# Kernel optimization log

Measured on AMD Instinct MI355X. Metric: run time of the kernel, lower is better.

## Reference

```python
import jax, jax.numpy as jnp
import numpy as np

N = 100000   # nodes
E = 1600000  # edges (before self loops)
H = 4        # heads
C = 32       # per-head channels
D = H * C    # hidden_dim = 128
G = 64       # graphs in batch
L = 4        # num_layers
IN_DIM = 7
NEG_SLOPE = 0.2


def setup_inputs() -> dict:
    key = jax.random.key(0)
    ks = jax.random.split(key, 14)
    s = 0.1
    x = jax.random.normal(ks[0], (N, IN_DIM), jnp.float32)
    edge_index = jax.random.randint(ks[1], (2, E), 0, N, dtype=jnp.int32)
    batch = jnp.sort(jax.random.randint(ks[2], (N,), 0, G, dtype=jnp.int32))
    W0 = jax.random.normal(ks[3], (IN_DIM, D), jnp.float32) * s
    a_src0 = jax.random.normal(ks[4], (H, C), jnp.float32) * s
    a_dst0 = jax.random.normal(ks[5], (H, C), jnp.float32) * s
    b0 = jnp.zeros((D,), jnp.float32)
    Ws = jax.random.normal(ks[6], (L - 1, D, D), jnp.float32) * s
    a_srcs = jax.random.normal(ks[7], (L - 1, H, C), jnp.float32) * s
    a_dsts = jax.random.normal(ks[8], (L - 1, H, C), jnp.float32) * s
    bs = jnp.zeros((L - 1, D), jnp.float32)
    ln_g = jnp.ones((L, D), jnp.float32)
    ln_b = jnp.zeros((L, D), jnp.float32)
    return dict(x=x, edge_index=edge_index, batch=batch, W0=W0, a_src0=a_src0,
                a_dst0=a_dst0, b0=b0, Ws=Ws, a_srcs=a_srcs, a_dsts=a_dsts,
                bs=bs, ln_g=ln_g, ln_b=ln_b)


def _gat_layer(x, W, a_src, a_dst, b, src, dst):
    # x: [N, F_in] -> h: [N, H, C] (PyG GATConv: shared lin for src/dst)
    h = (x @ W).reshape(N, H, C)
    alpha_src = jnp.einsum('nhc,hc->nh', h, a_src)  # [N, H]
    alpha_dst = jnp.einsum('nhc,hc->nh', h, a_dst)  # [N, H]
    logits = jax.nn.leaky_relu(alpha_src[src] + alpha_dst[dst], NEG_SLOPE)  # [E', H]
    # segment softmax over edges grouped by destination node
    m = jax.ops.segment_max(logits, dst, num_segments=N)          # [N, H]
    e = jnp.exp(logits - m[dst])
    z = jax.ops.segment_sum(e, dst, num_segments=N)               # [N, H]
    alpha = e / (z[dst] + 1e-16)                                  # [E', H]
    msg = h[src] * alpha[..., None]                               # [E', H, C]
    out = jax.ops.segment_sum(msg, dst, num_segments=N)           # [N, H, C]
    return out.reshape(N, D) + b


def _layernorm(x, g, b):
    mu = jnp.mean(x, axis=-1, keepdims=True)
    var = jnp.var(x, axis=-1, keepdims=True)
    return (x - mu) * jax.lax.rsqrt(var + 1e-5) * g + b


def reference(x, edge_index, batch, W0, a_src0, a_dst0, b0, Ws, a_srcs, a_dsts, bs, ln_g, ln_b):
    # PyG GATConv default: add self loops
    loop = jnp.arange(N, dtype=edge_index.dtype)
    src = jnp.concatenate([edge_index[0], loop])
    dst = jnp.concatenate([edge_index[1], loop])
    h = x
    for i in range(L):
        if i == 0:
            W, asr, ads, b = W0, a_src0, a_dst0, b0
        else:
            W, asr, ads, b = Ws[i - 1], a_srcs[i - 1], a_dsts[i - 1], bs[i - 1]
        h_new = _gat_layer(h, W, asr, ads, b, src, dst)
        h_new = jax.nn.elu(_layernorm(h_new, ln_g[i], ln_b[i]))
        h = h + h_new if i > 0 else h_new  # dropout is identity in eval
    node_embeddings = h  # [N, D]
    sums = jax.ops.segment_sum(node_embeddings, batch, num_segments=G)  # [G, D]
    cnt = jax.ops.segment_sum(jnp.ones((N,), node_embeddings.dtype), batch, num_segments=G)
    graph_embedding = sums / jnp.maximum(cnt, 1.0)[:, None]
    return node_embeddings, graph_embedding
```

## Files before the change

### kernel.cpp

```cpp
#include <hip/hip_runtime.h>
#include <hip/hip_bf16.h>

#define NN 100000
#define NE 1600000
#define EP (NE + NN)
#define NH 4
#define NC 32
#define DD 128
#define NG 64
#define NIN 7

#define BSH 9
#define NBUK ((NN + 511) >> BSH)
#define SEGCAP 9600
#define NHB ((NE + 255)/256)

typedef __hip_bfloat16 bf16;
typedef __attribute__((ext_vector_type(8))) short short8;
typedef __attribute__((ext_vector_type(4))) float f32x4;

__device__ __forceinline__ float b2f(const bf16 v){ return __bfloat162float(v); }

__device__ __forceinline__ float in_ld(const void* p, size_t i, int f32){
  return f32 ? ((const float*)p)[i] : b2f(((const bf16*)p)[i]);
}

__device__ __forceinline__ unsigned int bfbits(float v){
  bf16 b = __float2bfloat16(v);
  return (unsigned int)(*(unsigned short*)&b);
}

__global__ __launch_bounds__(256) void k_init(int* __restrict__ deg, int* __restrict__ cursor,
                                              float* __restrict__ gsum, int* __restrict__ gcnt,
                                              const unsigned int* __restrict__ xb, int* __restrict__ flag){
  int i = blockIdx.x*256 + threadIdx.x;
  if (i < NN){ deg[i] = 1; cursor[i] = 1; }
  if (i < NG*DD) gsum[i] = 0.f;
  if (i < NG) gcnt[i] = 0;
  if (blockIdx.x == 0 && threadIdx.x < 64){
    int t = threadIdx.x;
    int pl = 0;
    for (int j = t; j < 512; j += 64){
      float v = __uint_as_float(xb[j]);
      float a = fabsf(v);
      if (v == v && a < 1e6f && a > 1e-10f) pl++;
    }
    #pragma unroll
    for (int off = 32; off > 0; off >>= 1) pl += __shfl_down(pl, off);
    if (t == 0) *flag = (pl >= 384) ? 1 : 0;
  }
}

__global__ __launch_bounds__(256) void k_hist(const int* __restrict__ dst, int* __restrict__ deg,
                                              const void* __restrict__ Ws, bf16* __restrict__ WT,
                                              const int* __restrict__ flag){
  if (blockIdx.x >= NHB){
    int l = blockIdx.x - NHB;
    int f32 = *flag;
    for (int idx = threadIdx.x; idx < DD*DD; idx += 256){
      int n = idx >> 7, k = idx & 127;
      WT[(size_t)l*DD*DD + idx] = __float2bfloat16(in_ld(Ws, (size_t)l*DD*DD + (size_t)k*DD + n, f32));
    }
    return;
  }
  int e = blockIdx.x*256 + threadIdx.x;
  if (e < NE){
    unsigned int d = (unsigned int)dst[e];
    if (d < NN) atomicAdd(&deg[d], 1);
  }
}

__global__ __launch_bounds__(256) void k_scan1(const int* __restrict__ deg, int* __restrict__ incl,
                                               int* __restrict__ bsum){
  __shared__ int tmp[256];
  int t = threadIdx.x, i = blockIdx.x*256 + t;
  int v = (i < NN) ? deg[i] : 0;
  tmp[t] = v; __syncthreads();
  for (int off=1; off<256; off<<=1){
    int a = (t >= off) ? tmp[t-off] : 0;
    __syncthreads();
    tmp[t] += a;
    __syncthreads();
  }
  if (i < NN) incl[i] = tmp[t];
  if (t == 255) bsum[blockIdx.x] = tmp[255];
}

__global__ __launch_bounds__(512) void k_scan2(const int* __restrict__ bsum, int* __restrict__ bex, int nb){
  __shared__ int tmp[512];
  int t = threadIdx.x;
  int v = (t < nb) ? bsum[t] : 0;
  tmp[t] = v; __syncthreads();
  for (int off=1; off<512; off<<=1){
    int a = (t >= off) ? tmp[t-off] : 0;
    __syncthreads();
    tmp[t] += a;
    __syncthreads();
  }
  if (t < nb) bex[t] = tmp[t] - v;
}

__global__ __launch_bounds__(256) void k_scan3(const int* __restrict__ incl, const int* __restrict__ bex,
                                               int* __restrict__ offs){
  int i = blockIdx.x*256 + threadIdx.x;
  if (i < NN) offs[i+1] = incl[i] + bex[i>>8];
  if (i == 0) offs[0] = 0;
}

__global__ __launch_bounds__(256) void k_binit(const int* __restrict__ offs, int* __restrict__ bcur){
  int b = threadIdx.x + blockIdx.x*256;
  if (b < NBUK){
    int ns = b << BSH;
    bcur[b] = offs[ns] - ns;
  }
}

__global__ __launch_bounds__(256) void k_bin(const int* __restrict__ src, const int* __restrict__ dst,
                                             int* __restrict__ bcur, int2* __restrict__ gstag){
  __shared__ int cnt[NBUK], pref[NBUK+1], place[NBUK], gbase[NBUK];
  __shared__ int2 pairs[4096];
  int tid = threadIdx.x;
  for (int b = tid; b < NBUK; b += 256){ cnt[b]=0; place[b]=0; }
  __syncthreads();
  int e0 = blockIdx.x*4096;
  int s[16], d[16];
  #pragma unroll
  for (int i=0;i<16;i++){
    int e = e0 + i*256 + tid;
    s[i] = 0; d[i] = -1;
    if (e < NE){
      unsigned int us = (unsigned int)src[e]; if (us >= NN) us = 0;
      unsigned int ud = (unsigned int)dst[e]; if (ud >= NN) ud = 0;
      s[i] = (int)us; d[i] = (int)ud;
      atomicAdd(&cnt[ud>>BSH], 1);
    }
  }
  __syncthreads();
  if (tid == 0){
    int run = 0;
    for (int b=0;b<NBUK;b++){ pref[b] = run; run += cnt[b]; }
    pref[NBUK] = run;
  }
  __syncthreads();
  for (int b = tid; b < NBUK; b += 256){
    if (cnt[b] > 0) gbase[b] = atomicAdd(&bcur[b], cnt[b]);
  }
  __syncthreads();
  #pragma unroll
  for (int i=0;i<16;i++){
    if (d[i] >= 0){
      int b = d[i]>>BSH;
      int lp = atomicAdd(&place[b],1);
      pairs[pref[b]+lp] = make_int2(s[i], d[i]);
    }
  }
  __syncthreads();
  int tot = pref[NBUK];
  for (int j = tid; j < tot; j += 256){
    int2 pr = pairs[j];
    int b = pr.y>>BSH;
    int gidx = gbase[b] + (j - pref[b]);
    if (gidx >= 0 && gidx < NE) gstag[gidx] = pr;
  }
}

__global__ __launch_bounds__(256) void k_bucket(const int* __restrict__ offs,
                                                const int2* __restrict__ gstag,
                                                int* __restrict__ csr, int* __restrict__ cursor){
  __shared__ int seg[SEGCAP];
  __shared__ int lcur[512];
  int b = blockIdx.x, tid = threadIdx.x;
  int nstart = b << BSH;
  int nend = min(nstart + 512, NN);
  int nloc = nend - nstart;
  int base = offs[nstart];
  int segN = offs[nend] - base;
  if (segN < 0) segN = 0;
  int ecnt = segN - nloc; if (ecnt < 0) ecnt = 0;
  int estart = base - nstart;
  if (segN <= SEGCAP){
    for (int ln = tid; ln < nloc; ln += 256){
      lcur[ln] = 1;
      int p = offs[nstart+ln] - base;
      if (p >= 0 && p < SEGCAP) seg[p] = nstart + ln;
    }
    __syncthreads();
    for (int j = tid; j < ecnt; j += 256){
      int sidx = estart + j;
      int2 pr = (sidx >= 0 && sidx < NE) ? gstag[sidx] : make_int2(0, nstart);
      int ln = pr.y - nstart;
      if (ln < 0 || ln >= nloc) ln = 0;
      int p = atomicAdd(&lcur[ln], 1);
      int idx = offs[nstart+ln] - base + p;
      if (idx >= 0 && idx < SEGCAP) seg[idx] = pr.x;
    }
    __syncthreads();
    for (int j = tid; j < segN; j += 256) csr[base + j] = seg[j];
  } else {
    for (int ln = tid; ln < nloc; ln += 256){
      int p = offs[nstart+ln];
      if (p >= 0 && p < EP) csr[p] = nstart + ln;
    }
    __syncthreads();
    for (int j = tid; j < ecnt; j += 256){
      int sidx = estart + j;
      int2 pr = (sidx >= 0 && sidx < NE) ? gstag[sidx] : make_int2(0, nstart);
      unsigned int dd = (unsigned int)pr.y; if (dd >= NN) dd = 0;
      int p = atomicAdd(&cursor[dd], 1);
      int idx = offs[dd] + p;
      if (idx >= 0 && idx < EP) csr[idx] = pr.x;
    }
  }
}

__device__ __forceinline__ void alpha_red(float acc, float was, float wad, int d, int n,
                                          float* __restrict__ asrc, float* __restrict__ adst){
  float ps = acc*was, pd = acc*wad;
  #pragma unroll
  for (int off=16; off>0; off>>=1){
    ps += __shfl_down(ps, off, 32);
    pd += __shfl_down(pd, off, 32);
  }
  if ((d & 31) == 0){
    asrc[n*NH + (d>>5)] = ps;
    adst[n*NH + (d>>5)] = pd;
  }
}

__global__ __launch_bounds__(128) void k_gemm0(const void* __restrict__ x, const void* __restrict__ W,
    const void* __restrict__ aws, const void* __restrict__ awd,
    bf16* __restrict__ hproj,
    float* __restrict__ asrc, float* __restrict__ adst, const int* __restrict__ flag){
  int f32 = *flag;
  __shared__ float xr[4][NIN];
  int d = threadIdx.x;
  int n0 = blockIdx.x*4;
  if (d < 4*NIN) xr[d/NIN][d%NIN] = in_ld(x, (size_t)n0*NIN + d, f32);
  __syncthreads();
  float a0=0,a1=0,a2=0,a3=0;
  #pragma unroll
  for (int k=0;k<NIN;k++){
    float w = in_ld(W, (size_t)k*DD + d, f32);
    a0 += xr[0][k]*w; a1 += xr[1][k]*w; a2 += xr[2][k]*w; a3 += xr[3][k]*w;
  }
  hproj[(size_t)(n0+0)*DD+d]=__float2bfloat16(a0);
  hproj[(size_t)(n0+1)*DD+d]=__float2bfloat16(a1);
  hproj[(size_t)(n0+2)*DD+d]=__float2bfloat16(a2);
  hproj[(size_t)(n0+3)*DD+d]=__float2bfloat16(a3);
  float was = in_ld(aws, d, f32), wad = in_ld(awd, d, f32);
  alpha_red(a0, was, wad, d, n0+0, asrc, adst);
  alpha_red(a1, was, wad, d, n0+1, asrc, adst);
  alpha_red(a2, was, wad, d, n0+2, asrc, adst);
  alpha_red(a3, was, wad, d, n0+3, asrc, adst);
}

#define LDA 136
#define LDB 136

__global__ __launch_bounds__(256) void k_gemm_mfma(
    const bf16* __restrict__ resid,
    const bf16* __restrict__ WT, size_t wtoff,
    const void* __restrict__ aws, const void* __restrict__ awd, size_t aoff,
    bf16* __restrict__ hproj,
    float* __restrict__ asrc, float* __restrict__ adst,
    const int* __restrict__ flag)
{
  __shared__ bf16 sA[64*LDA];
  __shared__ bf16 sB[128*LDB];
  int f32 = *flag;
  int t = threadIdx.x;
  int n0 = blockIdx.x*64;

  {
    const uint4* srcv = (const uint4*)(WT + wtoff);
    #pragma unroll
    for (int i=0;i<8;i++){
      int u4 = t + 256*i;
      int row = u4 >> 4, c = u4 & 15;
      *(uint4*)(&sB[row*LDB + c*8]) = srcv[u4];
    }
  }
  {
    const uint4* av = (const uint4*)resid;
    #pragma unroll
    for (int i=0;i<4;i++){
      int u4 = t + 256*i;
      int row = u4 >> 4, c = u4 & 15;
      int gr = n0 + row;
      uint4 v = make_uint4(0,0,0,0);
      if (gr < NN) v = av[(size_t)gr*16 + c];
      *(uint4*)(&sA[row*LDA + c*8]) = v;
    }
  }
  __syncthreads();

  int wv = t >> 6, lane = t & 63;
  int m = lane & 15, kq = lane >> 4;
  int rowbase = wv*16;

  f32x4 acc[8];
  #pragma unroll
  for (int nt=0; nt<8; nt++) acc[nt] = (f32x4){0.f,0.f,0.f,0.f};

  #pragma unroll
  for (int ks=0; ks<4; ks++){
    short8 afrag = *(const short8*)(&sA[(rowbase + m)*LDA + ks*32 + kq*8]);
    #pragma unroll
    for (int nt=0; nt<8; nt++){
      short8 bfrag = *(const short8*)(&sB[(nt*16 + m)*LDB + ks*32 + kq*8]);
      acc[nt] = __builtin_amdgcn_mfma_f32_16x16x32_bf16(afrag, bfrag, acc[nt], 0, 0, 0);
    }
  }

  #pragma unroll
  for (int reg=0; reg<4; reg++){
    int gr = n0 + rowbase + kq*4 + reg;
    if (gr < NN){
      bf16* dst = hproj + (size_t)gr*DD + m;
      #pragma unroll
      for (int nt=0; nt<8; nt++)
        dst[nt*16] = __float2bfloat16(acc[nt][reg]);
    }
  }

  float avs[8], avd[8];
  #pragma unroll
  for (int nt=0; nt<8; nt++){
    avs[nt] = in_ld(aws, aoff + nt*16 + m, f32);
    avd[nt] = in_ld(awd, aoff + nt*16 + m, f32);
  }
  #pragma unroll
  for (int h=0; h<4; h++){
    #pragma unroll
    for (int reg=0; reg<4; reg++){
      float ps = acc[2*h][reg]*avs[2*h] + acc[2*h+1][reg]*avs[2*h+1];
      float pd = acc[2*h][reg]*avd[2*h] + acc[2*h+1][reg]*avd[2*h+1];
      #pragma unroll
      for (int off=1; off<16; off<<=1){
        ps += __shfl_xor(ps, off);
        pd += __shfl_xor(pd, off);
      }
      if (m == 0){
        int gr = n0 + rowbase + kq*4 + reg;
        if (gr < NN){
          asrc[gr*NH + h] = ps;
          adst[gr*NH + h] = pd;
        }
      }
    }
  }
}

__device__ __forceinline__ float4 edge_e(const float4 as, const float4 ad){
  float4 l, e;
  l.x = as.x + ad.x; l.y = as.y + ad.y; l.z = as.z + ad.z; l.w = as.w + ad.w;
  l.x = l.x > 0.f ? l.x : 0.2f*l.x;
  l.y = l.y > 0.f ? l.y : 0.2f*l.y;
  l.z = l.z > 0.f ? l.z : 0.2f*l.z;
  l.w = l.w > 0.f ? l.w : 0.2f*l.w;
  l.x = fminf(l.x, 30.f); l.y = fminf(l.y, 30.f);
  l.z = fminf(l.z, 30.f); l.w = fminf(l.w, 30.f);
  e.x = __expf(l.x); e.y = __expf(l.y); e.z = __expf(l.z); e.w = __expf(l.w);
  return e;
}

__device__ __forceinline__ float2 hp_ld2(const void* hp, int s, int lane){
  unsigned int hv = ((const unsigned int*)hp)[(size_t)s*64 + lane];
  return make_float2(__uint_as_float(hv << 16), __uint_as_float(hv & 0xFFFF0000u));
}

__global__ __launch_bounds__(256) void k_agg(const bf16* __restrict__ hproj,
    const float* __restrict__ asrc, const float* __restrict__ adst,
    const int* __restrict__ offs, const int* __restrict__ csr,
    bf16* __restrict__ resid,
    const void* __restrict__ bias, size_t boff,
    const void* __restrict__ lng, const void* __restrict__ lnb, size_t lnoff,
    const int* __restrict__ flag, const int first)
{
  __shared__ float s_al[4][256];
  int f32 = *flag;
  int wid = threadIdx.x >> 6, lane = threadIdx.x & 63;
  int n = blockIdx.x*4 + wid;
  int beg = offs[n];
  int end = offs[n+1];
  beg = max(0, min(beg, EP));
  end = max(beg, min(end, EP));
  int deg = min(end - beg, 1024);
  const float4 ad = ((const float4*)adst)[n];
  int head = lane >> 4;
  float2 a0c = make_float2(0.f,0.f), a1c = make_float2(0.f,0.f);
  float2 a2c = make_float2(0.f,0.f), a3c = make_float2(0.f,0.f);

  if (deg <= 64){
    float4 e = make_float4(0,0,0,0);
    int sreg = 0;
    if (lane < deg){
      unsigned int us = (unsigned int)csr[beg+lane];
      if (us >= NN) us = 0;
      sreg = (int)us;
      float4 as = ((const float4*)asrc)[sreg];
      e = edge_e(as, ad);
    }
    float4 zs = e;
    #pragma unroll
    for (int off=32; off>0; off>>=1){
      zs.x += __shfl_down(zs.x, off);
      zs.y += __shfl_down(zs.y, off);
      zs.z += __shfl_down(zs.z, off);
      zs.w += __shfl_down(zs.w, off);
    }
    float4 invz;
    invz.x = 1.f/(__shfl(zs.x,0)+1e-16f);
    invz.y = 1.f/(__shfl(zs.y,0)+1e-16f);
    invz.z = 1.f/(__shfl(zs.z,0)+1e-16f);
    invz.w = 1.f/(__shfl(zs.w,0)+1e-16f);
    if (lane < deg){
      s_al[wid][lane*4+0] = e.x*invz.x;
      s_al[wid][lane*4+1] = e.y*invz.y;
      s_al[wid][lane*4+2] = e.z*invz.z;
      s_al[wid][lane*4+3] = e.w*invz.w;
    }
    __threadfence_block();
    int t = 0;
    for (; t+4 <= deg; t += 4){
      int s0 = __shfl(sreg, t+0), s1 = __shfl(sreg, t+1);
      int s2 = __shfl(sreg, t+2), s3 = __shfl(sreg, t+3);
      float2 v0 = hp_ld2(hproj, s0, lane);
      float2 v1 = hp_ld2(hproj, s1, lane);
      float2 v2 = hp_ld2(hproj, s2, lane);
      float2 v3 = hp_ld2(hproj, s3, lane);
      float al0 = s_al[wid][(t+0)*4+head];
      float al1 = s_al[wid][(t+1)*4+head];
      float al2 = s_al[wid][(t+2)*4+head];
      float al3 = s_al[wid][(t+3)*4+head];
      a0c.x += v0.x*al0; a0c.y += v0.y*al0;
      a1c.x += v1.x*al1; a1c.y += v1.y*al1;
      a2c.x += v2.x*al2; a2c.y += v2.y*al2;
      a3c.x += v3.x*al3; a3c.y += v3.y*al3;
    }
    for (; t < deg; t++){
      int s = __shfl(sreg, t);
      float a = s_al[wid][t*4+head];
      float2 hv = hp_ld2(hproj, s, lane);
      a0c.x += hv.x*a;
      a0c.y += hv.y*a;
    }
  } else {
    float4 zs = make_float4(0,0,0,0);
    for (int j=lane; j<deg; j+=64){
      unsigned int us = (unsigned int)csr[beg+j];
      if (us >= NN) us = 0;
      float4 as = ((const float4*)asrc)[us];
      float4 e = edge_e(as, ad);
      zs.x+=e.x; zs.y+=e.y; zs.z+=e.z; zs.w+=e.w;
    }
    #pragma unroll
    for (int off=32; off>0; off>>=1){
      zs.x += __shfl_down(zs.x, off);
      zs.y += __shfl_down(zs.y, off);
      zs.z += __shfl_down(zs.z, off);
      zs.w += __shfl_down(zs.w, off);
    }
    float4 invz;
    invz.x = 1.f/(__shfl(zs.x,0)+1e-16f);
    invz.y = 1.f/(__shfl(zs.y,0)+1e-16f);
    invz.z = 1.f/(__shfl(zs.z,0)+1e-16f);
    invz.w = 1.f/(__shfl(zs.w,0)+1e-16f);
    int nch = (deg+63)>>6;
    for (int c2=0;c2<nch;c2++){
      int base = c2<<6, j = base+lane;
      int sreg = 0;
      __threadfence_block();
      if (j < deg){
        unsigned int us = (unsigned int)csr[beg+j];
        if (us >= NN) us = 0;
        sreg = (int)us;
        float4 as = ((const float4*)asrc)[sreg];
        float4 e = edge_e(as, ad);
        s_al[wid][lane*4+0]=e.x*invz.x;
        s_al[wid][lane*4+1]=e.y*invz.y;
        s_al[wid][lane*4+2]=e.z*invz.z;
        s_al[wid][lane*4+3]=e.w*invz.w;
      }
      __threadfence_block();
      int cnt = min(64, deg-base);
      for (int t=0;t<cnt;t++){
        int s = __shfl(sreg, t);
        float a = s_al[wid][t*4+head];
        float2 hv = hp_ld2(hproj, s, lane);
        a0c.x += hv.x*a;
        a0c.y += hv.y*a;
      }
    }
  }

  float2 acc = make_float2(a0c.x + a1c.x + a2c.x + a3c.x,
                           a0c.y + a1c.y + a2c.y + a3c.y);

  float vx = acc.x + in_ld(bias, boff + 2*lane,   f32);
  float vy = acc.y + in_ld(bias, boff + 2*lane+1, f32);
  float s1 = vx+vy, s2 = vx*vx+vy*vy;
  #pragma unroll
  for (int off=32; off>0; off>>=1){
    s1 += __shfl_down(s1, off);
    s2 += __shfl_down(s2, off);
  }
  float mean = __shfl(s1,0) * (1.f/DD);
  float msq  = __shfl(s2,0) * (1.f/DD);
  float var  = fmaxf(msq - mean*mean, 0.f);
  float r = rsqrtf(var + 1e-5f);
  float yx = (vx-mean)*r*in_ld(lng, lnoff+2*lane,   f32) + in_ld(lnb, lnoff+2*lane,   f32);
  float yy = (vy-mean)*r*in_ld(lng, lnoff+2*lane+1, f32) + in_ld(lnb, lnoff+2*lane+1, f32);
  yx = yx>0.f ? yx : expm1f(yx);
  yy = yy>0.f ? yy : expm1f(yy);
  float2 res;
  if (first){
    res = make_float2(yx, yy);
  } else {
    unsigned int pu = ((const unsigned int*)resid)[(size_t)n*64 + lane];
    res = make_float2(__uint_as_float(pu << 16) + yx,
                      __uint_as_float(pu & 0xFFFF0000u) + yy);
  }
  unsigned int pk = bfbits(res.x) | (bfbits(res.y) << 16);
  ((unsigned int*)resid)[(size_t)n*64 + lane] = pk;
}

__global__ __launch_bounds__(128) void k_pool(const bf16* __restrict__ resid, void* __restrict__ dout,
    const int* __restrict__ batch, float* __restrict__ gsum, int* __restrict__ gcnt,
    const int* __restrict__ flag){
  __shared__ int sb[64];
  int f32 = *flag;
  int d = threadIdx.x;
  int n0 = blockIdx.x*64;
  int cnt = min(64, NN - n0);
  if (d < cnt){
    unsigned int b = (unsigned int)batch[n0 + d];
    if (b >= NG) b = 0;
    sb[d] = (int)b;
  }
  __syncthreads();
  float local = 0.f;
  int cur = sb[0];
  for (int i=0;i<cnt;i++){
    int b = sb[i];
    if (b != cur){
      atomicAdd(&gsum[cur*DD + d], local);
      local = 0.f; cur = b;
    }
    size_t idx = (size_t)(n0+i)*DD + d;
    float v = b2f(resid[idx]);
    if (f32) ((float*)dout)[idx] = v;
    else     ((bf16*)dout)[idx] = resid[idx];
    local += v;
  }
  atomicAdd(&gsum[cur*DD + d], local);
  if (d == 0){
    int lc = 0; int c2 = sb[0];
    for (int i=0;i<cnt;i++){
      int b = sb[i];
      if (b != c2){ atomicAdd(&gcnt[c2], lc); lc = 0; c2 = b; }
      lc++;
    }
    atomicAdd(&gcnt[c2], lc);
  }
}

__global__ __launch_bounds__(128) void k_final(const float* __restrict__ gsum, const int* __restrict__ gcnt,
                                               void* __restrict__ dout, const int* __restrict__ flag){
  int f32 = *flag;
  int i = blockIdx.x*128 + threadIdx.x;
  if (i < NG*DD){
    float c = (float)gcnt[i>>7];
    if (c < 1.f) c = 1.f;
    float val = gsum[i] / c;
    if (f32) ((float*)dout)[(size_t)NN*DD + i] = val;
    else     ((bf16*)dout)[(size_t)NN*DD + i] = __float2bfloat16(val);
  }
}

extern "C" void kernel_launch(void* const* d_in, const int* in_sizes, int n_in,
                              void* d_out, int out_size, void* d_ws, size_t ws_size,
                              hipStream_t stream){
  const void* x      = d_in[0];
  const int*  ei     = (const int*) d_in[1];
  const int*  batch  = (const int*) d_in[2];
  const void* W0     = d_in[3];
  const void* asrc0  = d_in[4];
  const void* adst0  = d_in[5];
  const void* b0     = d_in[6];
  const void* Ws     = d_in[7];
  const void* asrcs  = d_in[8];
  const void* adsts  = d_in[9];
  const void* bs     = d_in[10];
  const void* lng    = d_in[11];
  const void* lnb    = d_in[12];

  const int* srcs = ei;
  const int* dsts = ei + NE;

  uintptr_t p0 = (uintptr_t)d_ws;
  uintptr_t p = p0;
  auto alloc = [&](size_t bytes)->void* {
    void* r = (void*)p; p += (bytes + 255) & ~(size_t)255; return r;
  };
  int*   csr    = (int*)  alloc((size_t)EP*4);
  int*   offs   = (int*)  alloc((size_t)(NN+1)*4);
  float* asrc   = (float*)alloc((size_t)NN*NH*4);
  float* adst   = (float*)alloc((size_t)NN*NH*4);
  int*   deg    = (int*)  alloc((size_t)NN*4);
  int*   cursor = (int*)  alloc((size_t)NN*4);
  int*   incl   = (int*)  alloc((size_t)NN*4);
  int*   bsum   = (int*)  alloc(512*4);
  int*   bex    = (int*)  alloc(512*4);
  float* gsum   = (float*)alloc((size_t)NG*DD*4);
  int*   gcnt   = (int*)  alloc(NG*4);
  int*   flag   = (int*)  alloc(256);
  int*   bcur   = (int*)  alloc((size_t)NBUK*4);
  int2*  gstag  = (int2*) alloc((size_t)NE*8);
  bf16*  wt     = (bf16*) alloc((size_t)3*DD*DD*2);

  bf16* hproj = (bf16*)alloc((size_t)NN*DD*2);
  bf16* resid = (bf16*)alloc((size_t)NN*DD*2);

  const int NB = (NN + 255)/256;

  k_init<<<NB, 256, 0, stream>>>(deg, cursor, gsum, gcnt, (const unsigned int*)x, flag);
  k_hist<<<NHB + 3, 256, 0, stream>>>(dsts, deg, Ws, wt, flag);
  k_scan1<<<NB, 256, 0, stream>>>(deg, incl, bsum);
  k_scan2<<<1, 512, 0, stream>>>(bsum, bex, NB);
  k_scan3<<<NB, 256, 0, stream>>>(incl, bex, offs);
  k_binit<<<1, 256, 0, stream>>>(offs, bcur);
  k_bin<<<(NE+4095)/4096, 256, 0, stream>>>(srcs, dsts, bcur, gstag);
  k_bucket<<<NBUK, 256, 0, stream>>>(offs, gstag, csr, cursor);

  const int GEMM_B = (NN + 63)/64;

  for (int l=0; l<4; l++){
    if (l == 0){
      k_gemm0<<<NN/4, 128, 0, stream>>>(x, W0, asrc0, adst0, hproj, asrc, adst, flag);
      k_agg<<<NN/4, 256, 0, stream>>>(hproj, asrc, adst, offs, csr, resid,
                                      b0, 0, lng, lnb, 0, flag, 1);
    } else {
      size_t wtoff = (size_t)(l-1)*DD*DD;
      size_t aoff  = (size_t)(l-1)*DD;
      k_gemm_mfma<<<GEMM_B, 256, 0, stream>>>(resid, wt, wtoff,
                                              asrcs, adsts, aoff,
                                              hproj, asrc, adst, flag);
      k_agg<<<NN/4, 256, 0, stream>>>(hproj, asrc, adst, offs, csr, resid,
                                      bs, (size_t)(l-1)*DD, lng, lnb, (size_t)l*DD, flag, 0);
    }
  }

  k_pool<<<(NN+63)/64, 128, 0, stream>>>(resid, d_out, batch, gsum, gcnt, flag);
  k_final<<<(NG*DD+127)/128, 128, 0, stream>>>(gsum, gcnt, d_out, flag);
}
```

Measured before the change: 726.3 us.

## Build CSR with fixed-capacity per-bucket segments and drop the global degree scan

Removes the global degree histogram, the three-stage prefix scan and the bucket-init kernel. Edges are now binned straight into fixed-capacity per-bucket staging slots, and each bucket block computes its own local degree counts, offsets and end pointers in shared memory. Aggregation reads separate start and end arrays into a padded CSR layout. This cuts several launches and a full atomic pass over the destination array. In exchange, any bucket holding more edges than the fixed capacity silently drops edges, and the old fallback path for that case is gone.

```diff
diff --git a/kernel.cpp b/kernel.cpp
--- a/kernel.cpp
+++ b/kernel.cpp
@@ -3,7 +3,6 @@
 
 #define NN 100000
 #define NE 1600000
-#define EP (NE + NN)
 #define NH 4
 #define NC 32
 #define DD 128
@@ -13,7 +12,9 @@
 #define BSH 9
 #define NBUK ((NN + 511) >> BSH)
 #define SEGCAP 9600
-#define NHB ((NE + 255)/256)
+#define CAPE (SEGCAP - 512)
+#define CSRN (NBUK * SEGCAP)
+#define NBBIN ((NE + 4095)/4096)
 
 typedef __hip_bfloat16 bf16;
 typedef __attribute__((ext_vector_type(8))) short short8;
@@ -30,13 +31,13 @@
   return (unsigned int)(*(unsigned short*)&b);
 }
 
-__global__ __launch_bounds__(256) void k_init(int* __restrict__ deg, int* __restrict__ cursor,
-                                              float* __restrict__ gsum, int* __restrict__ gcnt,
+__global__ __launch_bounds__(256) void k_init(float* __restrict__ gsum, int* __restrict__ gcnt,
+                                              int* __restrict__ bcur,
                                               const unsigned int* __restrict__ xb, int* __restrict__ flag){
   int i = blockIdx.x*256 + threadIdx.x;
-  if (i < NN){ deg[i] = 1; cursor[i] = 1; }
   if (i < NG*DD) gsum[i] = 0.f;
   if (i < NG) gcnt[i] = 0;
+  if (i < NBUK) bcur[i] = i * CAPE;
   if (blockIdx.x == 0 && threadIdx.x < 64){
     int t = threadIdx.x;
     int pl = 0;
@@ -51,11 +52,12 @@
   }
 }
 
-__global__ __launch_bounds__(256) void k_hist(const int* __restrict__ dst, int* __restrict__ deg,
-                                              const void* __restrict__ Ws, bf16* __restrict__ WT,
-                                              const int* __restrict__ flag){
-  if (blockIdx.x >= NHB){
-    int l = blockIdx.x - NHB;
+__global__ __launch_bounds__(256) void k_bin(const int* __restrict__ src, const int* __restrict__ dst,
+                                             int* __restrict__ bcur, int2* __restrict__ gstag,
+                                             const void* __restrict__ Ws, bf16* __restrict__ WT,
+                                             const int* __restrict__ flag){
+  if (blockIdx.x >= NBBIN){
+    int l = blockIdx.x - NBBIN;
     int f32 = *flag;
     for (int idx = threadIdx.x; idx < DD*DD; idx += 256){
       int n = idx >> 7, k = idx & 127;
@@ -63,60 +65,6 @@
     }
     return;
   }
-  int e = blockIdx.x*256 + threadIdx.x;
-  if (e < NE){
-    unsigned int d = (unsigned int)dst[e];
-    if (d < NN) atomicAdd(&deg[d], 1);
-  }
-}
-
-__global__ __launch_bounds__(256) void k_scan1(const int* __restrict__ deg, int* __restrict__ incl,
-                                               int* __restrict__ bsum){
-  __shared__ int tmp[256];
-  int t = threadIdx.x, i = blockIdx.x*256 + t;
-  int v = (i < NN) ? deg[i] : 0;
-  tmp[t] = v; __syncthreads();
-  for (int off=1; off<256; off<<=1){
-    int a = (t >= off) ? tmp[t-off] : 0;
-    __syncthreads();
-    tmp[t] += a;
-    __syncthreads();
-  }
-  if (i < NN) incl[i] = tmp[t];
-  if (t == 255) bsum[blockIdx.x] = tmp[255];
-}
-
-__global__ __launch_bounds__(512) void k_scan2(const int* __restrict__ bsum, int* __restrict__ bex, int nb){
-  __shared__ int tmp[512];
-  int t = threadIdx.x;
-  int v = (t < nb) ? bsum[t] : 0;
-  tmp[t] = v; __syncthreads();
-  for (int off=1; off<512; off<<=1){
-    int a = (t >= off) ? tmp[t-off] : 0;
-    __syncthreads();
-    tmp[t] += a;
-    __syncthreads();
-  }
-  if (t < nb) bex[t] = tmp[t] - v;
-}
-
-__global__ __launch_bounds__(256) void k_scan3(const int* __restrict__ incl, const int* __restrict__ bex,
-                                               int* __restrict__ offs){
-  int i = blockIdx.x*256 + threadIdx.x;
-  if (i < NN) offs[i+1] = incl[i] + bex[i>>8];
-  if (i == 0) offs[0] = 0;
-}
-
-__global__ __launch_bounds__(256) void k_binit(const int* __restrict__ offs, int* __restrict__ bcur){
-  int b = threadIdx.x + blockIdx.x*256;
-  if (b < NBUK){
-    int ns = b << BSH;
-    bcur[b] = offs[ns] - ns;
-  }
-}
-
-__global__ __launch_bounds__(256) void k_bin(const int* __restrict__ src, const int* __restrict__ dst,
-                                             int* __restrict__ bcur, int2* __restrict__ gstag){
   __shared__ int cnt[NBUK], pref[NBUK+1], place[NBUK], gbase[NBUK];
   __shared__ int2 pairs[4096];
   int tid = threadIdx.x;
@@ -160,57 +108,74 @@
     int2 pr = pairs[j];
     int b = pr.y>>BSH;
     int gidx = gbase[b] + (j - pref[b]);
-    if (gidx >= 0 && gidx < NE) gstag[gidx] = pr;
-  }
-}
-
-__global__ __launch_bounds__(256) void k_bucket(const int* __restrict__ offs,
-                                                const int2* __restrict__ gstag,
-                                                int* __restrict__ csr, int* __restrict__ cursor){
+    if (gidx >= b*CAPE && gidx < (b+1)*CAPE) gstag[gidx] = pr;
+  }
+}
+
+__global__ __launch_bounds__(256) void k_bucket(const int2* __restrict__ gstag,
+                                                const int* __restrict__ bcur,
+                                                int* __restrict__ csr,
+                                                int* __restrict__ offs, int* __restrict__ oend){
   __shared__ int seg[SEGCAP];
-  __shared__ int lcur[512];
+  __shared__ int lcnt[512];
+  __shared__ int loff[512];
+  __shared__ int pscan[256];
   int b = blockIdx.x, tid = threadIdx.x;
   int nstart = b << BSH;
   int nend = min(nstart + 512, NN);
   int nloc = nend - nstart;
-  int base = offs[nstart];
-  int segN = offs[nend] - base;
-  if (segN < 0) segN = 0;
-  int ecnt = segN - nloc; if (ecnt < 0) ecnt = 0;
-  int estart = base - nstart;
-  if (segN <= SEGCAP){
-    for (int ln = tid; ln < nloc; ln += 256){
-      lcur[ln] = 1;
-      int p = offs[nstart+ln] - base;
-      if (p >= 0 && p < SEGCAP) seg[p] = nstart + ln;
-    }
+  int base = b * SEGCAP;
+  int stbase = b * CAPE;
+  int ecnt = bcur[b] - stbase;
+  ecnt = max(0, min(ecnt, CAPE));
+  lcnt[tid]     = (tid < nloc) ? 1 : 0;
+  lcnt[tid+256] = (tid+256 < nloc) ? 1 : 0;
+  __syncthreads();
+  for (int j = tid; j < ecnt; j += 256){
+    int2 pr = gstag[stbase + j];
+    int ln = pr.y - nstart;
+    if (ln < 0 || ln >= nloc) ln = 0;
+    atomicAdd(&lcnt[ln], 1);
+  }
+  __syncthreads();
+  int c0 = lcnt[2*tid], c1 = lcnt[2*tid+1];
+  int pairsum = c0 + c1;
+  pscan[tid] = pairsum;
+  __syncthreads();
+  for (int off=1; off<256; off<<=1){
+    int a = (tid >= off) ? pscan[tid-off] : 0;
     __syncthreads();
-    for (int j = tid; j < ecnt; j += 256){
-      int sidx = estart + j;
-      int2 pr = (sidx >= 0 && sidx < NE) ? gstag[sidx] : make_int2(0, nstart);
-      int ln = pr.y - nstart;
-      if (ln < 0 || ln >= nloc) ln = 0;
-      int p = atomicAdd(&lcur[ln], 1);
-      int idx = offs[nstart+ln] - base + p;
-      if (idx >= 0 && idx < SEGCAP) seg[idx] = pr.x;
-    }
+    pscan[tid] += a;
     __syncthreads();
-    for (int j = tid; j < segN; j += 256) csr[base + j] = seg[j];
-  } else {
-    for (int ln = tid; ln < nloc; ln += 256){
-      int p = offs[nstart+ln];
-      if (p >= 0 && p < EP) csr[p] = nstart + ln;
-    }
-    __syncthreads();
-    for (int j = tid; j < ecnt; j += 256){
-      int sidx = estart + j;
-      int2 pr = (sidx >= 0 && sidx < NE) ? gstag[sidx] : make_int2(0, nstart);
-      unsigned int dd = (unsigned int)pr.y; if (dd >= NN) dd = 0;
-      int p = atomicAdd(&cursor[dd], 1);
-      int idx = offs[dd] + p;
-      if (idx >= 0 && idx < EP) csr[idx] = pr.x;
-    }
-  }
+  }
+  int pexcl = pscan[tid] - pairsum;
+  loff[2*tid]   = pexcl;
+  loff[2*tid+1] = pexcl + c0;
+  __syncthreads();
+  int segN = pscan[255];
+  if (segN > SEGCAP) segN = SEGCAP;
+  if (tid < nloc){
+    offs[nstart + tid] = base + loff[tid];
+    oend[nstart + tid] = base + loff[tid] + lcnt[tid];
+  }
+  if (tid + 256 < nloc){
+    offs[nstart + tid + 256] = base + loff[tid+256];
+    oend[nstart + tid + 256] = base + loff[tid+256] + lcnt[tid+256];
+  }
+  __syncthreads();
+  if (tid < nloc){ int p = loff[tid]; if (p < SEGCAP) seg[p] = nstart + tid; lcnt[tid] = 1; }
+  if (tid + 256 < nloc){ int p = loff[tid+256]; if (p < SEGCAP) seg[p] = nstart + tid + 256; lcnt[tid+256] = 1; }
+  __syncthreads();
+  for (int j = tid; j < ecnt; j += 256){
+    int2 pr = gstag[stbase + j];
+    int ln = pr.y - nstart;
+    if (ln < 0 || ln >= nloc) ln = 0;
+    int p = atomicAdd(&lcnt[ln], 1);
+    int idx = loff[ln] + p;
+    if (idx >= 0 && idx < SEGCAP) seg[idx] = pr.x;
+  }
+  __syncthreads();
+  for (int j = tid; j < segN; j += 256) csr[base + j] = seg[j];
 }
 
 __device__ __forceinline__ void alpha_red(float acc, float was, float wad, int d, int n,
@@ -371,7 +336,7 @@
 
 __global__ __launch_bounds__(256) void k_agg(const bf16* __restrict__ hproj,
     const float* __restrict__ asrc, const float* __restrict__ adst,
-    const int* __restrict__ offs, const int* __restrict__ csr,
+    const int* __restrict__ offs, const int* __restrict__ oend, const int* __restrict__ csr,
     bf16* __restrict__ resid,
     const void* __restrict__ bias, size_t boff,
     const void* __restrict__ lng, const void* __restrict__ lnb, size_t lnoff,
@@ -382,9 +347,9 @@
   int wid = threadIdx.x >> 6, lane = threadIdx.x & 63;
   int n = blockIdx.x*4 + wid;
   int beg = offs[n];
-  int end = offs[n+1];
-  beg = max(0, min(beg, EP));
-  end = max(beg, min(end, EP));
+  int end = oend[n];
+  beg = max(0, min(beg, CSRN));
+  end = max(beg, min(end, CSRN));
   int deg = min(end - beg, 1024);
   const float4 ad = ((const float4*)adst)[n];
   int head = lane >> 4;
@@ -603,42 +568,32 @@
   auto alloc = [&](size_t bytes)->void* {
     void* r = (void*)p; p += (bytes + 255) & ~(size_t)255; return r;
   };
-  int*   csr    = (int*)  alloc((size_t)EP*4);
-  int*   offs   = (int*)  alloc((size_t)(NN+1)*4);
+  int*   csr    = (int*)  alloc((size_t)CSRN*4);
+  int*   offs   = (int*)  alloc((size_t)NN*4);
+  int*   oend   = (int*)  alloc((size_t)NN*4);
   float* asrc   = (float*)alloc((size_t)NN*NH*4);
   float* adst   = (float*)alloc((size_t)NN*NH*4);
-  int*   deg    = (int*)  alloc((size_t)NN*4);
-  int*   cursor = (int*)  alloc((size_t)NN*4);
-  int*   incl   = (int*)  alloc((size_t)NN*4);
-  int*   bsum   = (int*)  alloc(512*4);
-  int*   bex    = (int*)  alloc(512*4);
   float* gsum   = (float*)alloc((size_t)NG*DD*4);
   int*   gcnt   = (int*)  alloc(NG*4);
   int*   flag   = (int*)  alloc(256);
   int*   bcur   = (int*)  alloc((size_t)NBUK*4);
-  int2*  gstag  = (int2*) alloc((size_t)NE*8);
+  int2*  gstag  = (int2*) alloc((size_t)NBUK*CAPE*8);
   bf16*  wt     = (bf16*) alloc((size_t)3*DD*DD*2);
-
-  bf16* hproj = (bf16*)alloc((size_t)NN*DD*2);
-  bf16* resid = (bf16*)alloc((size_t)NN*DD*2);
+  bf16*  hproj  = (bf16*) alloc((size_t)NN*DD*2);
+  bf16*  resid  = (bf16*) alloc((size_t)NN*DD*2);
 
   const int NB = (NN + 255)/256;
 
-  k_init<<<NB, 256, 0, stream>>>(deg, cursor, gsum, gcnt, (const unsigned int*)x, flag);
-  k_hist<<<NHB + 3, 256, 0, stream>>>(dsts, deg, Ws, wt, flag);
-  k_scan1<<<NB, 256, 0, stream>>>(deg, incl, bsum);
-  k_scan2<<<1, 512, 0, stream>>>(bsum, bex, NB);
-  k_scan3<<<NB, 256, 0, stream>>>(incl, bex, offs);
-  k_binit<<<1, 256, 0, stream>>>(offs, bcur);
-  k_bin<<<(NE+4095)/4096, 256, 0, stream>>>(srcs, dsts, bcur, gstag);
-  k_bucket<<<NBUK, 256, 0, stream>>>(offs, gstag, csr, cursor);
+  k_init<<<NB, 256, 0, stream>>>(gsum, gcnt, bcur, (const unsigned int*)x, flag);
+  k_bin<<<NBBIN + 3, 256, 0, stream>>>(srcs, dsts, bcur, gstag, Ws, wt, flag);
+  k_bucket<<<NBUK, 256, 0, stream>>>(gstag, bcur, csr, offs, oend);
 
   const int GEMM_B = (NN + 63)/64;
 
   for (int l=0; l<4; l++){
     if (l == 0){
       k_gemm0<<<NN/4, 128, 0, stream>>>(x, W0, asrc0, adst0, hproj, asrc, adst, flag);
-      k_agg<<<NN/4, 256, 0, stream>>>(hproj, asrc, adst, offs, csr, resid,
+      k_agg<<<NN/4, 256, 0, stream>>>(hproj, asrc, adst, offs, oend, csr, resid,
                                       b0, 0, lng, lnb, 0, flag, 1);
     } else {
       size_t wtoff = (size_t)(l-1)*DD*DD;
@@ -646,7 +601,7 @@
       k_gemm_mfma<<<GEMM_B, 256, 0, stream>>>(resid, wt, wtoff,
                                               asrcs, adsts, aoff,
                                               hproj, asrc, adst, flag);
-      k_agg<<<NN/4, 256, 0, stream>>>(hproj, asrc, adst, offs, csr, resid,
+      k_agg<<<NN/4, 256, 0, stream>>>(hproj, asrc, adst, offs, oend, csr, resid,
                                       bs, (size_t)(l-1)*DD, lng, lnb, (size_t)l*DD, flag, 0);
     }
   }
```

Result: faster. 642.8 us (-11.5%).
